# Performance work log

Hardware: AMD Instinct MI355X
Metric: run time of the kernel (lower is better)

The kernel has to match this reference:

```python
import jax, jax.numpy as jnp
import numpy as np

EPS = 1e-6
MAX_RATIO = 1e6
CLAMP_ABS = 1e6

def _sanitize(x):
    x = jnp.nan_to_num(x, nan=0.0, posinf=CLAMP_ABS, neginf=-CLAMP_ABS)
    return jnp.clip(x, -CLAMP_ABS, CLAMP_ABS)

def setup_inputs() -> dict:
    key = jax.random.key(0)
    gaussians = jax.random.normal(key, (32, 65536, 14), dtype=jnp.float32)
    return {"gaussians": gaussians}

def reference(gaussians) -> jnp.ndarray:
    pos = gaussians[..., 0:3]                      # [B, N, 3]
    N = pos.shape[1]
    pc = pos - jnp.mean(pos, axis=1, keepdims=True)  # center per batch
    cov = jnp.einsum('bni,bnj->bij', pc, pc) / N     # [B, 3, 3]
    cov = _sanitize(cov)
    cov = 0.5 * (cov + jnp.swapaxes(cov, -1, -2))    # symmetrize
    eig = jnp.linalg.eigvalsh(cov)                   # ascending, [B, 3]
    max_e = jnp.clip(_sanitize(eig[..., -1]), EPS, None)
    min_e = jnp.clip(_sanitize(eig[..., 0]), EPS, None)
    ratio = jnp.clip(max_e / min_e, 1.0, MAX_RATIO)
    return -jnp.mean(jnp.log(ratio))
```

## Files before the change

kernel.cpp:

```cpp
#include <hip/hip_runtime.h>
#include <math.h>

#define BATCHES 32
#define NPTS 65536
#define CH 14
#define BLOCKS_PER_BATCH 32
#define THREADS 256
#define PPB (NPTS / BLOCKS_PER_BATCH)

__global__ __launch_bounds__(THREADS) void moments_kernel(
    const float* __restrict__ g, double* __restrict__ ws) {
    const int b   = blockIdx.x / BLOCKS_PER_BATCH;
    const int blk = blockIdx.x % BLOCKS_PER_BATCH;
    const size_t base_pt = (size_t)b * NPTS + (size_t)blk * PPB;

    float sx = 0.f, sy = 0.f, sz = 0.f;
    float sxx = 0.f, syy = 0.f, szz = 0.f;
    float sxy = 0.f, sxz = 0.f, syz = 0.f;

    for (int i = threadIdx.x; i < PPB; i += THREADS) {
        const float* p = g + (base_pt + (size_t)i) * CH;
        float2 xy = *(const float2*)p;
        float z = p[2];
        float x = xy.x, y = xy.y;
        sx += x;    sy += y;    sz += z;
        sxx += x*x; syy += y*y; szz += z*z;
        sxy += x*y; sxz += x*z; syz += y*z;
    }

    float vals[9] = {sx, sy, sz, sxx, syy, szz, sxy, sxz, syz};
#pragma unroll
    for (int k = 0; k < 9; ++k) {
        float v = vals[k];
#pragma unroll
        for (int off = 32; off >= 1; off >>= 1)
            v += __shfl_down(v, off, 64);
        vals[k] = v;
    }

    __shared__ float red[THREADS / 64][9];
    const int wave = threadIdx.x >> 6;
    const int lane = threadIdx.x & 63;
    if (lane == 0) {
#pragma unroll
        for (int k = 0; k < 9; ++k) red[wave][k] = vals[k];
    }
    __syncthreads();
    if (threadIdx.x == 0) {
#pragma unroll
        for (int k = 0; k < 9; ++k) {
            float s = red[0][k] + red[1][k] + red[2][k] + red[3][k];
            atomicAdd(&ws[b * 9 + k], (double)s);
        }
    }
}

__global__ __launch_bounds__(64) void finish_kernel(
    const double* __restrict__ ws, float* __restrict__ out) {
    __shared__ double logs[BATCHES];
    const int b = threadIdx.x;
    if (b < BATCHES) {
        const double* s = ws + b * 9;
        const double invN = 1.0 / (double)NPTS;
        double mx = s[0] * invN, my = s[1] * invN, mz = s[2] * invN;
        double a00 = s[3] * invN - mx * mx;
        double a11 = s[4] * invN - my * my;
        double a22 = s[5] * invN - mz * mz;
        double a01 = s[6] * invN - mx * my;
        double a02 = s[7] * invN - mx * mz;
        double a12 = s[8] * invN - my * mz;
        const double CL = 1e6;
        a00 = fmin(fmax(a00, -CL), CL); a11 = fmin(fmax(a11, -CL), CL);
        a22 = fmin(fmax(a22, -CL), CL); a01 = fmin(fmax(a01, -CL), CL);
        a02 = fmin(fmax(a02, -CL), CL); a12 = fmin(fmax(a12, -CL), CL);

        double q  = (a00 + a11 + a22) / 3.0;
        double p1 = a01 * a01 + a02 * a02 + a12 * a12;
        double b00 = a00 - q, b11 = a11 - q, b22 = a22 - q;
        double p2 = b00 * b00 + b11 * b11 + b22 * b22 + 2.0 * p1;
        double eigmax, eigmin;
        if (p2 <= 0.0) {
            eigmax = eigmin = q;
        } else {
            double p  = sqrt(p2 / 6.0);
            double ip = 1.0 / p;
            double c00 = b00 * ip, c11 = b11 * ip, c22 = b22 * ip;
            double c01 = a01 * ip, c02 = a02 * ip, c12 = a12 * ip;
            double detB = c00 * (c11 * c22 - c12 * c12)
                        - c01 * (c01 * c22 - c12 * c02)
                        + c02 * (c01 * c12 - c11 * c02);
            double r = detB * 0.5;
            r = fmin(1.0, fmax(-1.0, r));
            double phi = acos(r) / 3.0;
            eigmax = q + 2.0 * p * cos(phi);
            eigmin = q + 2.0 * p * cos(phi + 2.0943951023931953);
        }
        double maxe = fmax(fmin(eigmax, 1e6), 1e-6);
        double mine = fmax(fmin(eigmin, 1e6), 1e-6);
        double ratio = maxe / mine;
        ratio = fmin(fmax(ratio, 1.0), 1e6);
        logs[b] = log(ratio);
    }
    __syncthreads();
    if (threadIdx.x == 0) {
        double acc = 0.0;
#pragma unroll
        for (int i = 0; i < BATCHES; ++i) acc += logs[i];
        out[0] = (float)(-acc / (double)BATCHES);
    }
}

extern "C" void kernel_launch(void* const* d_in, const int* in_sizes, int n_in,
                              void* d_out, int out_size, void* d_ws, size_t ws_size,
                              hipStream_t stream) {
    const float* g = (const float*)d_in[0];
    float* out = (float*)d_out;
    double* ws = (double*)d_ws;

    hipMemsetAsync(ws, 0, BATCHES * 9 * sizeof(double), stream);

    moments_kernel<<<BATCHES * BLOCKS_PER_BATCH, THREADS, 0, stream>>>(g, ws);
    finish_kernel<<<1, 64, 0, stream>>>(ws, out);
}
```

Baseline: 172.7 us.

## Stage point tiles through LDS with coalesced float4 loads and drop atomics

Replaces strided per-record loads of xyz with cooperative float4 copies of whole 512-record tiles into shared memory, then each thread reads xyz from LDS. Per-block partial sums are written to a float workspace and reduced in the finish kernel, removing the memset and double atomics. This trades extra bytes loaded per record and LDS pressure (lower occupancy, two barriers per tile) for fully coalesced, wide global transactions.

```diff
diff --git a/kernel.cpp b/kernel.cpp
--- a/kernel.cpp
+++ b/kernel.cpp
@@ -7,25 +7,40 @@
 #define BLOCKS_PER_BATCH 32
 #define THREADS 256
 #define PPB (NPTS / BLOCKS_PER_BATCH)
+#define TILE_RECS 512
+#define TILE_FLOATS (TILE_RECS * CH)
+#define NTILES (PPB / TILE_RECS)
 
 __global__ __launch_bounds__(THREADS) void moments_kernel(
-    const float* __restrict__ g, double* __restrict__ ws) {
+    const float* __restrict__ g, float* __restrict__ ws) {
     const int b   = blockIdx.x / BLOCKS_PER_BATCH;
     const int blk = blockIdx.x % BLOCKS_PER_BATCH;
     const size_t base_pt = (size_t)b * NPTS + (size_t)blk * PPB;
+
+    __shared__ float buf[TILE_FLOATS];
 
     float sx = 0.f, sy = 0.f, sz = 0.f;
     float sxx = 0.f, syy = 0.f, szz = 0.f;
     float sxy = 0.f, sxz = 0.f, syz = 0.f;
 
-    for (int i = threadIdx.x; i < PPB; i += THREADS) {
-        const float* p = g + (base_pt + (size_t)i) * CH;
-        float2 xy = *(const float2*)p;
-        float z = p[2];
-        float x = xy.x, y = xy.y;
-        sx += x;    sy += y;    sz += z;
-        sxx += x*x; syy += y*y; szz += z*z;
-        sxy += x*y; sxz += x*z; syz += y*z;
+    for (int tile = 0; tile < NTILES; ++tile) {
+        const float4* src = (const float4*)(g + (base_pt + (size_t)tile * TILE_RECS) * CH);
+        float4* dst = (float4*)buf;
+#pragma unroll
+        for (int j = 0; j < TILE_FLOATS / 4 / THREADS; ++j) {
+            dst[threadIdx.x + j * THREADS] = src[threadIdx.x + j * THREADS];
+        }
+        __syncthreads();
+#pragma unroll
+        for (int j = 0; j < TILE_RECS / THREADS; ++j) {
+            const int r = threadIdx.x + j * THREADS;
+            const float* p = buf + r * CH;
+            float x = p[0], y = p[1], z = p[2];
+            sx += x;    sy += y;    sz += z;
+            sxx += x*x; syy += y*y; szz += z*z;
+            sxy += x*y; sxz += x*z; syz += y*z;
+        }
+        __syncthreads();
     }
 
     float vals[9] = {sx, sy, sz, sxx, syy, szz, sxy, sxz, syz};
@@ -49,18 +64,22 @@
     if (threadIdx.x == 0) {
 #pragma unroll
         for (int k = 0; k < 9; ++k) {
-            float s = red[0][k] + red[1][k] + red[2][k] + red[3][k];
-            atomicAdd(&ws[b * 9 + k], (double)s);
+            ws[blockIdx.x * 9 + k] = red[0][k] + red[1][k] + red[2][k] + red[3][k];
         }
     }
 }
 
 __global__ __launch_bounds__(64) void finish_kernel(
-    const double* __restrict__ ws, float* __restrict__ out) {
+    const float* __restrict__ ws, float* __restrict__ out) {
     __shared__ double logs[BATCHES];
     const int b = threadIdx.x;
     if (b < BATCHES) {
-        const double* s = ws + b * 9;
+        double s[9] = {0, 0, 0, 0, 0, 0, 0, 0, 0};
+        for (int blk = 0; blk < BLOCKS_PER_BATCH; ++blk) {
+            const float* p = ws + (b * BLOCKS_PER_BATCH + blk) * 9;
+#pragma unroll
+            for (int k = 0; k < 9; ++k) s[k] += (double)p[k];
+        }
         const double invN = 1.0 / (double)NPTS;
         double mx = s[0] * invN, my = s[1] * invN, mz = s[2] * invN;
         double a00 = s[3] * invN - mx * mx;
@@ -115,9 +134,7 @@
                               hipStream_t stream) {
     const float* g = (const float*)d_in[0];
     float* out = (float*)d_out;
-    double* ws = (double*)d_ws;
-
-    hipMemsetAsync(ws, 0, BATCHES * 9 * sizeof(double), stream);
+    float* ws = (float*)d_ws;
 
     moments_kernel<<<BATCHES * BLOCKS_PER_BATCH, THREADS, 0, stream>>>(g, ws);
     finish_kernel<<<1, 64, 0, stream>>>(ws, out);
```

Measured after the change: 174.7 us. Within noise of the previous version (+1.2%).
